# Optimization experiments

Hardware: AMD Instinct MI355X
Metric: run time of the kernel (lower is better)

## Reference

```python
import jax, jax.numpy as jnp
import numpy as np

EPS = 1e-5  # eqx.nn.LayerNorm default


def _layer_norm(x, w, b):
    m = x.mean(-1, keepdims=True)
    v = ((x - m) ** 2).mean(-1, keepdims=True)
    return (x - m) / jnp.sqrt(v + EPS) * w + b


def _s4_block(x, nw, nb, lre, lim, bre, bim, cre, cim, d, lstep, ow, ob, o2w, o2b):
    # x: [L, H]. One SequenceBlock: LayerNorm -> S4 recurrence (lax.scan) -> GELU -> GLU-style gated linear -> residual.
    skip = x
    h = _layer_norm(x, nw, nb)
    Lam = lre + 1j * lim                      # [H, N] complex diagonal state matrix
    step = jnp.exp(lstep)[:, None]            # [H, 1] per-channel timescale
    BL = 1.0 / (1.0 - (step / 2.0) * Lam)     # bilinear discretization
    Abar = BL * (1.0 + (step / 2.0) * Lam)    # [H, N]
    Bbar = BL * step * (bre + 1j * bim)       # [H, N]
    C = cre + 1j * cim                        # [H, N]

    def scan_fn(state, u):                    # state: [H, N] complex, u: [H]
        new = Abar * state + Bbar * u[:, None]
        y = 2.0 * jnp.sum(C * new, axis=-1).real + d * u
        return new, y

    init = jnp.zeros(Abar.shape, Abar.dtype)  # cell.init_state
    _, y = jax.lax.scan(scan_fn, init, h)     # [L, H]
    y = jax.nn.gelu(y)
    y = (y @ ow.T + ob) * jax.nn.sigmoid(y @ o2w.T + o2b)
    return skip + y


def setup_inputs() -> dict:
    key = jax.random.key(0)
    L, IN, OUT, H, N, NL = 2048, 4, 3, 512, 32, 4
    ks = jax.random.split(key, 16)
    return {
        "x": jax.random.normal(ks[0], (L, IN), jnp.float32),
        "enc_w": jax.random.normal(ks[1], (H, IN), jnp.float32) / np.sqrt(IN),
        "enc_b": jnp.zeros((H,), jnp.float32),
        "dec_w": jax.random.normal(ks[2], (OUT, H), jnp.float32) / np.sqrt(H),
        "dec_b": jnp.zeros((OUT,), jnp.float32),
        "norm_w": jnp.ones((NL, H), jnp.float32),
        "norm_b": jnp.zeros((NL, H), jnp.float32),
        "lam_re": -0.5 - jax.random.uniform(ks[3], (NL, H, N), jnp.float32),  # stable (Re < 0)
        "lam_im": np.pi * jax.random.normal(ks[4], (NL, H, N), jnp.float32),
        "b_re": jax.random.normal(ks[5], (NL, H, N), jnp.float32) / np.sqrt(N),
        "b_im": jax.random.normal(ks[6], (NL, H, N), jnp.float32) / np.sqrt(N),
        "c_re": jax.random.normal(ks[7], (NL, H, N), jnp.float32) / np.sqrt(N),
        "c_im": jax.random.normal(ks[8], (NL, H, N), jnp.float32) / np.sqrt(N),
        "d": jax.random.normal(ks[9], (NL, H), jnp.float32),
        "log_step": float(np.log(1e-3)) + float(np.log(1e-1) - np.log(1e-3)) * jax.random.uniform(ks[10], (NL, H), jnp.float32),
        "out_w": jax.random.normal(ks[11], (NL, H, H), jnp.float32) / np.sqrt(H),
        "out_b": jnp.zeros((NL, H), jnp.float32),
        "out2_w": jax.random.normal(ks[12], (NL, H, H), jnp.float32) / np.sqrt(H),
        "out2_b": jnp.zeros((NL, H), jnp.float32),
    }


def reference(x, enc_w, enc_b, dec_w, dec_b, norm_w, norm_b, lam_re, lam_im, b_re, b_im, c_re, c_im, d, log_step, out_w, out_b, out2_w, out2_b):
    h = x @ enc_w.T + enc_b                   # encoder: [L, IN] -> [L, H]
    for i in range(norm_w.shape[0]):          # fixed small n_layers loop
        h = _s4_block(h, norm_w[i], norm_b[i], lam_re[i], lam_im[i], b_re[i], b_im[i],
                      c_re[i], c_im[i], d[i], log_step[i], out_w[i], out_b[i], out2_w[i], out2_b[i])
    return h @ dec_w.T + dec_b                # decoder: [L, H] -> [L, OUT]
```

## Files before the change

kernel.cpp:

```cpp
#include <hip/hip_runtime.h>
#include <hip/hip_bf16.h>
#include <math.h>

#define LSEQ 2048
#define HD   512
#define NST  32
#define LC   32
#define NCHK 64
#define HH   (HD * HD)
#define NTHR 256

typedef __bf16 bf16;
typedef __bf16 bf16x8 __attribute__((ext_vector_type(8)));
typedef float  floatx4 __attribute__((ext_vector_type(4)));

__device__ __forceinline__ float wave_reduce_add(float v) {
#pragma unroll
    for (int m = 32; m; m >>= 1) v += __shfl_xor(v, m, 64);
    return v;
}

__device__ __forceinline__ float gelu_tanh(float x) {
    float z = 0.7978845608028654f * (x + 0.044715f * x * x * x);
    float e = __expf(2.f * z);
    float th = 1.f - 2.f / (e + 1.f);
    return 0.5f * x * (1.f + th);
}

__device__ __forceinline__ void make_ab(float lre, float lim, float step,
                                        float br0, float bi0,
                                        float& ar, float& ai, float& br, float& bi) {
    float s2 = 0.5f * step;
    float dr = 1.f - s2 * lre, di = -s2 * lim;
    float inv = 1.f / (dr * dr + di * di);
    float blr = dr * inv, bli = -di * inv;
    float nr = 1.f + s2 * lre, ni = s2 * lim;
    ar = blr * nr - bli * ni;
    ai = blr * ni + bli * nr;
    float tr = step * br0, ti = step * bi0;
    br = blr * tr - bli * ti;
    bi = blr * ti + bli * tr;
}

__global__ __launch_bounds__(256) void setup_kernel(
    const float* __restrict__ x,   const float* __restrict__ ew,
    const float* __restrict__ eb,  const float* __restrict__ ow,
    const float* __restrict__ o2w,
    const float* __restrict__ lre, const float* __restrict__ lim,
    const float* __restrict__ bre, const float* __restrict__ bim,
    const float* __restrict__ cre, const float* __restrict__ cim,
    const float* __restrict__ ls,
    float* __restrict__ h, bf16* __restrict__ wb,
    float2* __restrict__ cA, float2* __restrict__ cB,
    float2* __restrict__ cC, float2* __restrict__ cAp) {
    int bid = blockIdx.x, tid = threadIdx.x;
    if (bid < 4096) {
        int idx = bid * 256 + tid;
        int t = idx >> 9, i = idx & (HD - 1);
        float4 xv = *(const float4*)(x + t * 4);
        float4 wv = *(const float4*)(ew + i * 4);
        float acc = eb[i];
        acc = fmaf(xv.x, wv.x, acc); acc = fmaf(xv.y, wv.y, acc);
        acc = fmaf(xv.z, wv.z, acc); acc = fmaf(xv.w, wv.w, acc);
        h[idx] = acc;
    } else if (bid < 5120) {
        int b2 = bid - 4096;
        const float* src = (b2 >= 512) ? o2w : ow;
        bf16* dst = wb + (b2 >= 512 ? 4 * HH : 0);
        int i = ((b2 & 511) * 256 + tid) * 8;
        float4 a = *(const float4*)(src + i);
        float4 b = *(const float4*)(src + i + 4);
        bf16x8 o;
        o[0] = (bf16)a.x; o[1] = (bf16)a.y; o[2] = (bf16)a.z; o[3] = (bf16)a.w;
        o[4] = (bf16)b.x; o[5] = (bf16)b.y; o[6] = (bf16)b.z; o[7] = (bf16)b.w;
        *(bf16x8*)(dst + i) = o;
    } else {
        int tg = (bid - 5120) * 256 + tid;
        int lay = tg >> 14, rem = tg & 16383;
        int ch = rem >> 5, n = rem & 31;
        float step = __expf(ls[lay * HD + ch]);
        float ar, ai, br, bi;
        make_ab(lre[tg], lim[tg], step, bre[tg], bim[tg], ar, ai, br, bi);
        float xr = ar, xi = ai;
#pragma unroll
        for (int q = 0; q < 5; ++q) { float tt = xr * xr - xi * xi; xi = 2.f * xr * xi; xr = tt; }
        int dst = (lay * NST + n) * HD + ch;
        cA[dst]  = make_float2(ar, ai);
        cB[dst]  = make_float2(br, bi);
        cC[dst]  = make_float2(2.f * cre[tg], 2.f * cim[tg]);
        cAp[dst] = make_float2(xr, xi);
    }
}

__global__ __launch_bounds__(256) void lnstat_kernel(
    const float* __restrict__ h, float2* __restrict__ stats) {
    int wv = threadIdx.x >> 6, lane = threadIdx.x & 63;
    int row = blockIdx.x * 4 + wv;
    const float* hp = h + (size_t)row * HD + lane * 8;
    float v[8];
    *(float4*)(v)     = *(const float4*)(hp);
    *(float4*)(v + 4) = *(const float4*)(hp + 4);
    float s = 0.f;
#pragma unroll
    for (int e = 0; e < 8; ++e) s += v[e];
    s = wave_reduce_add(s);
    float m = s * (1.f / HD);
    float q = 0.f;
#pragma unroll
    for (int e = 0; e < 8; ++e) { float d = v[e] - m; q += d * d; }
    q = wave_reduce_add(q);
    float rstd = rsqrtf(q * (1.f / HD) + 1e-5f);
    if (lane == 0) stats[row] = make_float2(m, rstd);
}

__device__ __forceinline__ void load_norm_tile(
    float* tile, const float* __restrict__ h, const float2* __restrict__ stats,
    const float* __restrict__ nwp, const float* __restrict__ nbp,
    int bx, int by, int tid) {
    const float* ub = h + (size_t)(by * 4 * LC) * HD + bx * 16;
    const float2* st = stats + by * 4 * LC;
    const float* wp = nwp + bx * 16;
    const float* bp = nbp + bx * 16;
#pragma unroll
    for (int r = 0; r < 2; ++r) {
        int i = r * NTHR + tid;
        int tr = i >> 2, c4 = (i & 3) * 4;
        float4 hv = *(const float4*)(ub + (size_t)tr * HD + c4);
        float2 s2 = st[tr];
        float4 gv = *(const float4*)(wp + c4);
        float4 bv = *(const float4*)(bp + c4);
        float4 o;
        o.x = (hv.x - s2.x) * s2.y * gv.x + bv.x;
        o.y = (hv.y - s2.x) * s2.y * gv.y + bv.y;
        o.z = (hv.z - s2.x) * s2.y * gv.z + bv.z;
        o.w = (hv.w - s2.x) * s2.y * gv.w + bv.w;
        *(float4*)(tile + tr * 16 + c4) = o;
    }
}

__global__ __launch_bounds__(256, 2) void p1_kernel(
    const float* __restrict__ h, const float2* __restrict__ stats,
    const float* __restrict__ nwp, const float* __restrict__ nbp,
    const float2* __restrict__ cA, const float2* __restrict__ cB,
    float2* __restrict__ f, int lay) {
    __shared__ float tile[4 * LC * 16];
    int tid = threadIdx.x;
    int lane = tid & 63, w = tid >> 6;
    int chl = lane & 15, sub = lane >> 4;
    int bx = blockIdx.x, by = blockIdx.y;
    int ch = bx * 16 + chl;
    int chunk = by * 4 + w;
    load_norm_tile(tile, h, stats, nwp, nbp, bx, by, tid);
    int cbase = (lay * NST + sub * 8) * HD + ch;
    float aR[8], aI[8], bR[8], bI[8];
#pragma unroll
    for (int j = 0; j < 8; ++j) {
        float2 t = cA[cbase + j * HD]; aR[j] = t.x; aI[j] = t.y;
        t = cB[cbase + j * HD];        bR[j] = t.x; bI[j] = t.y;
    }
    float sr[8], si[8];
#pragma unroll
    for (int j = 0; j < 8; ++j) { sr[j] = 0.f; si[j] = 0.f; }
    __syncthreads();
    const float* tp = tile + (w * LC) * 16 + chl;
#pragma unroll 4
    for (int t = 0; t < LC; ++t) {
        float uu = tp[t * 16];
#pragma unroll
        for (int j = 0; j < 8; ++j) {
            float nr = fmaf(aR[j], sr[j], fmaf(-aI[j], si[j], bR[j] * uu));
            float ni = fmaf(aI[j], sr[j], fmaf( aR[j], si[j], bI[j] * uu));
            sr[j] = nr; si[j] = ni;
        }
    }
    float2* fp = f + (size_t)(chunk * NST + sub * 8) * HD + ch;
#pragma unroll
    for (int j = 0; j < 8; ++j) fp[(size_t)j * HD] = make_float2(sr[j], si[j]);
}

__global__ __launch_bounds__(256) void p2_kernel(
    float2* __restrict__ f, const float2* __restrict__ cAp, int lay) {
    int tg = blockIdx.x * 256 + threadIdx.x;
    int ch = tg & 511, n = tg >> 9;
    float2 ap = cAp[(lay * NST + n) * HD + ch];
    float2* fp = f + (size_t)n * HD + ch;
    const size_t cs = (size_t)NST * HD;
    float sr = 0.f, si = 0.f;
#pragma unroll 8
    for (int c = 0; c < NCHK; ++c) {
        float2 v = fp[c * cs];
        float nr = fmaf(ap.x, sr, fmaf(-ap.y, si, v.x));
        float ni = fmaf(ap.y, sr, fmaf( ap.x, si, v.y));
        sr = nr; si = ni;
        fp[c * cs] = make_float2(sr, si);
    }
}

__global__ __launch_bounds__(256, 2) void p3_kernel(
    const float* __restrict__ h, const float2* __restrict__ stats,
    const float* __restrict__ nwp, const float* __restrict__ nbp,
    const float2* __restrict__ f,
    const float2* __restrict__ cA, const float2* __restrict__ cB,
    const float2* __restrict__ cC, const float* __restrict__ d_p,
    bf16* __restrict__ g, int lay) {
    __shared__ float tile[4 * LC * 16];
    int tid = threadIdx.x;
    int lane = tid & 63, w = tid >> 6;
    int chl = lane & 15, sub = lane >> 4;
    int bx = blockIdx.x, by = blockIdx.y;
    int ch = bx * 16 + chl;
    int chunk = by * 4 + w;
    load_norm_tile(tile, h, stats, nwp, nbp, bx, by, tid);
    int cbase = (lay * NST + sub * 8) * HD + ch;
    float aR[8], aI[8], bR[8], bI[8], cR[8], cI[8];
#pragma unroll
    for (int j = 0; j < 8; ++j) {
        float2 t = cA[cbase + j * HD]; aR[j] = t.x; aI[j] = t.y;
        t = cB[cbase + j * HD];        bR[j] = t.x; bI[j] = t.y;
        t = cC[cbase + j * HD];        cR[j] = t.x; cI[j] = t.y;
    }
    float dch = d_p[lay * HD + ch];
    float sr[8], si[8];
    if (chunk > 0) {
        const float2* ip = f + (size_t)((chunk - 1) * NST + sub * 8) * HD + ch;
#pragma unroll
        for (int j = 0; j < 8; ++j) { float2 v = ip[(size_t)j * HD]; sr[j] = v.x; si[j] = v.y; }
    } else {
#pragma unroll
        for (int j = 0; j < 8; ++j) { sr[j] = 0.f; si[j] = 0.f; }
    }
    __syncthreads();
    const float* tp = tile + (w * LC) * 16 + chl;
    bf16* gp = g + (size_t)chunk * LC * HD + ch;
#pragma unroll 4
    for (int t = 0; t < LC; ++t) {
        float uu = tp[t * 16];
        float p = 0.f;
#pragma unroll
        for (int j = 0; j < 8; ++j) {
            float nr = fmaf(aR[j], sr[j], fmaf(-aI[j], si[j], bR[j] * uu));
            float ni = fmaf(aI[j], sr[j], fmaf( aR[j], si[j], bI[j] * uu));
            sr[j] = nr; si[j] = ni;
            p = fmaf(cR[j], nr, fmaf(-cI[j], ni, p));
        }
        p += __shfl_xor(p, 16);
        p += __shfl_xor(p, 32);
        float y = fmaf(dch, uu, p);
        if (sub == 0) gp[(size_t)t * HD] = (bf16)gelu_tanh(y);
    }
}

__global__ __launch_bounds__(256, 2) void mm_kernel(
    const bf16* __restrict__ A,
    const bf16* __restrict__ W1,
    const bf16* __restrict__ W2,
    const float* __restrict__ bias1, const float* __restrict__ bias2,
    float* __restrict__ Hio) {
    const int w = threadIdx.x >> 6, lane = threadIdx.x & 63;
    const int wm = w >> 1, wn = w & 1;
    const int bm = blockIdx.x >> 4, bn = blockIdx.x & 15;
    const int mW = bm * 64 + wm * 32;
    const int nW = bn * 32 + wn * 16;
    const int lrow = lane & 15, quad = lane >> 4;

    floatx4 acc1[2] = {{0.f,0.f,0.f,0.f},{0.f,0.f,0.f,0.f}};
    floatx4 acc2[2] = {{0.f,0.f,0.f,0.f},{0.f,0.f,0.f,0.f}};
    for (int k0 = 0; k0 < HD; k0 += 32) {
        int kk = k0 + quad * 8;
        bf16x8 a0 = *(const bf16x8*)(A + (size_t)(mW + lrow) * HD + kk);
        bf16x8 a1 = *(const bf16x8*)(A + (size_t)(mW + 16 + lrow) * HD + kk);
        bf16x8 p0 = *(const bf16x8*)(W1 + (size_t)(nW + lrow) * HD + kk);
        bf16x8 q0 = *(const bf16x8*)(W2 + (size_t)(nW + lrow) * HD + kk);
        acc1[0] = __builtin_amdgcn_mfma_f32_16x16x32_bf16(a0, p0, acc1[0], 0, 0, 0);
        acc1[1] = __builtin_amdgcn_mfma_f32_16x16x32_bf16(a1, p0, acc1[1], 0, 0, 0);
        acc2[0] = __builtin_amdgcn_mfma_f32_16x16x32_bf16(a0, q0, acc2[0], 0, 0, 0);
        acc2[1] = __builtin_amdgcn_mfma_f32_16x16x32_bf16(a1, q0, acc2[1], 0, 0, 0);
    }
    int jj = nW + lrow;
    float bb1 = bias1[jj], bb2 = bias2[jj];
#pragma unroll
    for (int fm = 0; fm < 2; ++fm)
#pragma unroll
        for (int r = 0; r < 4; ++r) {
            int t = mW + fm * 16 + quad * 4 + r;
            float z1 = acc1[fm][r] + bb1;
            float z2 = acc2[fm][r] + bb2;
            Hio[(size_t)t * HD + jj] += z1 / (1.f + __expf(-z2));
        }
}

__global__ __launch_bounds__(192) void dec_kernel(
    const float* __restrict__ h, const float* __restrict__ w,
    const float* __restrict__ b, float* __restrict__ out) {
    int j = threadIdx.x >> 6, lane = threadIdx.x & 63;
    int t = blockIdx.x;
    const float* hp = h + (size_t)t * HD + lane * 8;
    float v[8];
    *(float4*)(v)     = *(const float4*)(hp);
    *(float4*)(v + 4) = *(const float4*)(hp + 4);
    float w8[8];
    *(float4*)(w8)     = *(const float4*)(w + j * HD + lane * 8);
    *(float4*)(w8 + 4) = *(const float4*)(w + j * HD + lane * 8 + 4);
    float s = 0.f;
#pragma unroll
    for (int e = 0; e < 8; ++e) s = fmaf(v[e], w8[e], s);
    s = wave_reduce_add(s);
    if (lane == 0) out[t * 3 + j] = s + b[j];
}

extern "C" void kernel_launch(void* const* d_in, const int* in_sizes, int n_in,
                              void* d_out, int out_size, void* d_ws, size_t ws_size,
                              hipStream_t stream) {
    const float* x   = (const float*)d_in[0];
    const float* ew  = (const float*)d_in[1];
    const float* eb  = (const float*)d_in[2];
    const float* dw  = (const float*)d_in[3];
    const float* db  = (const float*)d_in[4];
    const float* nw  = (const float*)d_in[5];
    const float* nb  = (const float*)d_in[6];
    const float* lre = (const float*)d_in[7];
    const float* lim = (const float*)d_in[8];
    const float* bre = (const float*)d_in[9];
    const float* bim = (const float*)d_in[10];
    const float* cre = (const float*)d_in[11];
    const float* cim = (const float*)d_in[12];
    const float* dd  = (const float*)d_in[13];
    const float* ls  = (const float*)d_in[14];
    const float* ow  = (const float*)d_in[15];
    const float* ob  = (const float*)d_in[16];
    const float* o2w = (const float*)d_in[17];
    const float* o2b = (const float*)d_in[18];

    char* ws = (char*)d_ws;
    float*  h     = (float*)ws;
    float2* f     = (float2*)(ws + (4  << 20));
    bf16*   g     = (bf16*)(ws + (16 << 20));
    bf16*   wb    = (bf16*)(ws + (18 << 20));
    float2* cA    = (float2*)(ws + (22 << 20));
    float2* cB    = (float2*)(ws + (22 << 20) + (512 << 10));
    float2* cC    = (float2*)(ws + (23 << 20));
    float2* cAp   = (float2*)(ws + (23 << 20) + (512 << 10));
    float2* stats = (float2*)(ws + (24 << 20));

    setup_kernel<<<5376, 256, 0, stream>>>(x, ew, eb, ow, o2w,
                                           lre, lim, bre, bim, cre, cim, ls,
                                           h, wb, cA, cB, cC, cAp);
    for (int lay = 0; lay < 4; ++lay) {
        int oH = lay * HD;
        lnstat_kernel<<<LSEQ / 4, 256, 0, stream>>>(h, stats);
        p1_kernel<<<dim3(HD / 16, NCHK / 4), 256, 0, stream>>>(
            h, stats, nw + oH, nb + oH, cA, cB, f, lay);
        p2_kernel<<<64, 256, 0, stream>>>(f, cAp, lay);
        p3_kernel<<<dim3(HD / 16, NCHK / 4), 256, 0, stream>>>(
            h, stats, nw + oH, nb + oH, f, cA, cB, cC, dd, g, lay);
        mm_kernel<<<512, 256, 0, stream>>>(
            g, wb + lay * HH, wb + 4 * HH + lay * HH, ob + oH, o2b + oH, h);
    }
    dec_kernel<<<LSEQ, 192, 0, stream>>>(h, dw, db, (float*)d_out);
}
```

Measured before the change: 305.6 us.

## Fuse LayerNorm statistics into producer epilogues and prefetch p2 chunk loads

```diff
diff --git a/kernel.cpp b/kernel.cpp
--- a/kernel.cpp
+++ b/kernel.cpp
@@ -13,12 +13,6 @@
 typedef __bf16 bf16;
 typedef __bf16 bf16x8 __attribute__((ext_vector_type(8)));
 typedef float  floatx4 __attribute__((ext_vector_type(4)));
-
-__device__ __forceinline__ float wave_reduce_add(float v) {
-#pragma unroll
-    for (int m = 32; m; m >>= 1) v += __shfl_xor(v, m, 64);
-    return v;
-}
 
 __device__ __forceinline__ float gelu_tanh(float x) {
     float z = 0.7978845608028654f * (x + 0.044715f * x * x * x);
@@ -52,17 +46,25 @@
     const float* __restrict__ ls,
     float* __restrict__ h, bf16* __restrict__ wb,
     float2* __restrict__ cA, float2* __restrict__ cB,
-    float2* __restrict__ cC, float2* __restrict__ cAp) {
+    float2* __restrict__ cC, float2* __restrict__ cAp,
+    float2* __restrict__ statP) {
     int bid = blockIdx.x, tid = threadIdx.x;
     if (bid < 4096) {
         int idx = bid * 256 + tid;
-        int t = idx >> 9, i = idx & (HD - 1);
+        int t = idx >> 9, col = idx & (HD - 1);
         float4 xv = *(const float4*)(x + t * 4);
-        float4 wv = *(const float4*)(ew + i * 4);
-        float acc = eb[i];
+        float4 wv = *(const float4*)(ew + col * 4);
+        float acc = eb[col];
         acc = fmaf(xv.x, wv.x, acc); acc = fmaf(xv.y, wv.y, acc);
         acc = fmaf(xv.z, wv.z, acc); acc = fmaf(xv.w, wv.w, acc);
         h[idx] = acc;
+        float s = acc, s2 = acc * acc;
+#pragma unroll
+        for (int m = 1; m <= 8; m <<= 1) {
+            s  += __shfl_xor(s, m, 64);
+            s2 += __shfl_xor(s2, m, 64);
+        }
+        if ((tid & 15) == 0) statP[(size_t)t * 32 + (col >> 4)] = make_float2(s, s2);
     } else if (bid < 5120) {
         int b2 = bid - 4096;
         const float* src = (b2 >= 512) ? o2w : ow;
@@ -92,33 +94,25 @@
     }
 }
 
-__global__ __launch_bounds__(256) void lnstat_kernel(
-    const float* __restrict__ h, float2* __restrict__ stats) {
-    int wv = threadIdx.x >> 6, lane = threadIdx.x & 63;
-    int row = blockIdx.x * 4 + wv;
-    const float* hp = h + (size_t)row * HD + lane * 8;
-    float v[8];
-    *(float4*)(v)     = *(const float4*)(hp);
-    *(float4*)(v + 4) = *(const float4*)(hp + 4);
-    float s = 0.f;
-#pragma unroll
-    for (int e = 0; e < 8; ++e) s += v[e];
-    s = wave_reduce_add(s);
-    float m = s * (1.f / HD);
-    float q = 0.f;
-#pragma unroll
-    for (int e = 0; e < 8; ++e) { float d = v[e] - m; q += d * d; }
-    q = wave_reduce_add(q);
-    float rstd = rsqrtf(q * (1.f / HD) + 1e-5f);
-    if (lane == 0) stats[row] = make_float2(m, rstd);
-}
-
-__device__ __forceinline__ void load_norm_tile(
-    float* tile, const float* __restrict__ h, const float2* __restrict__ stats,
+__device__ __forceinline__ void stats_and_tile(
+    float* tile, float2* stat_s,
+    const float* __restrict__ h, const float2* __restrict__ statP,
     const float* __restrict__ nwp, const float* __restrict__ nbp,
     int bx, int by, int tid) {
+    if (tid < 128) {
+        const float4* pp = (const float4*)(statP + (size_t)(by * 128 + tid) * 32);
+        float S = 0.f, S2 = 0.f;
+#pragma unroll
+        for (int k = 0; k < 16; ++k) {
+            float4 v = pp[k];
+            S += v.x + v.z; S2 += v.y + v.w;
+        }
+        float m = S * (1.f / HD);
+        float var = S2 * (1.f / HD) - m * m;
+        stat_s[tid] = make_float2(m, rsqrtf(var + 1e-5f));
+    }
+    __syncthreads();
     const float* ub = h + (size_t)(by * 4 * LC) * HD + bx * 16;
-    const float2* st = stats + by * 4 * LC;
     const float* wp = nwp + bx * 16;
     const float* bp = nbp + bx * 16;
 #pragma unroll
@@ -126,7 +120,7 @@
         int i = r * NTHR + tid;
         int tr = i >> 2, c4 = (i & 3) * 4;
         float4 hv = *(const float4*)(ub + (size_t)tr * HD + c4);
-        float2 s2 = st[tr];
+        float2 s2 = stat_s[tr];
         float4 gv = *(const float4*)(wp + c4);
         float4 bv = *(const float4*)(bp + c4);
         float4 o;
@@ -139,18 +133,19 @@
 }
 
 __global__ __launch_bounds__(256, 2) void p1_kernel(
-    const float* __restrict__ h, const float2* __restrict__ stats,
+    const float* __restrict__ h, const float2* __restrict__ statP,
     const float* __restrict__ nwp, const float* __restrict__ nbp,
     const float2* __restrict__ cA, const float2* __restrict__ cB,
     float2* __restrict__ f, int lay) {
     __shared__ float tile[4 * LC * 16];
+    __shared__ float2 stat_s[128];
     int tid = threadIdx.x;
     int lane = tid & 63, w = tid >> 6;
     int chl = lane & 15, sub = lane >> 4;
     int bx = blockIdx.x, by = blockIdx.y;
     int ch = bx * 16 + chl;
     int chunk = by * 4 + w;
-    load_norm_tile(tile, h, stats, nwp, nbp, bx, by, tid);
+    stats_and_tile(tile, stat_s, h, statP, nwp, nbp, bx, by, tid);
     int cbase = (lay * NST + sub * 8) * HD + ch;
     float aR[8], aI[8], bR[8], bI[8];
 #pragma unroll
@@ -184,33 +179,45 @@
     int ch = tg & 511, n = tg >> 9;
     float2 ap = cAp[(lay * NST + n) * HD + ch];
     float2* fp = f + (size_t)n * HD + ch;
-    const size_t cs = (size_t)NST * HD;
+    const size_t CS = (size_t)NST * HD;
+    float2 cur[8], nxt[8];
+#pragma unroll
+    for (int k = 0; k < 8; ++k) cur[k] = fp[(size_t)k * CS];
     float sr = 0.f, si = 0.f;
-#pragma unroll 8
-    for (int c = 0; c < NCHK; ++c) {
-        float2 v = fp[c * cs];
-        float nr = fmaf(ap.x, sr, fmaf(-ap.y, si, v.x));
-        float ni = fmaf(ap.y, sr, fmaf( ap.x, si, v.y));
-        sr = nr; si = ni;
-        fp[c * cs] = make_float2(sr, si);
+#pragma unroll
+    for (int b = 0; b < 8; ++b) {
+        if (b < 7) {
+#pragma unroll
+            for (int k = 0; k < 8; ++k) nxt[k] = fp[(size_t)(b * 8 + 8 + k) * CS];
+        }
+#pragma unroll
+        for (int k = 0; k < 8; ++k) {
+            float nr = fmaf(ap.x, sr, fmaf(-ap.y, si, cur[k].x));
+            float ni = fmaf(ap.y, sr, fmaf( ap.x, si, cur[k].y));
+            sr = nr; si = ni;
+            fp[(size_t)(b * 8 + k) * CS] = make_float2(sr, si);
+        }
+#pragma unroll
+        for (int k = 0; k < 8; ++k) cur[k] = nxt[k];
     }
 }
 
 __global__ __launch_bounds__(256, 2) void p3_kernel(
-    const float* __restrict__ h, const float2* __restrict__ stats,
+    const float* __restrict__ h, const float2* __restrict__ statP,
     const float* __restrict__ nwp, const float* __restrict__ nbp,
     const float2* __restrict__ f,
     const float2* __restrict__ cA, const float2* __restrict__ cB,
     const float2* __restrict__ cC, const float* __restrict__ d_p,
     bf16* __restrict__ g, int lay) {
     __shared__ float tile[4 * LC * 16];
+    __shared__ float2 stat_s[128];
     int tid = threadIdx.x;
     int lane = tid & 63, w = tid >> 6;
     int chl = lane & 15, sub = lane >> 4;
     int bx = blockIdx.x, by = blockIdx.y;
     int ch = bx * 16 + chl;
     int chunk = by * 4 + w;
-    load_norm_tile(tile, h, stats, nwp, nbp, bx, by, tid);
+    stats_and_tile(tile, stat_s, h, statP, nwp, nbp, bx, by, tid);
     int cbase = (lay * NST + sub * 8) * HD + ch;
     float aR[8], aI[8], bR[8], bI[8], cR[8], cI[8];
 #pragma unroll
@@ -255,7 +262,7 @@
     const bf16* __restrict__ W1,
     const bf16* __restrict__ W2,
     const float* __restrict__ bias1, const float* __restrict__ bias2,
-    float* __restrict__ Hio) {
+    float* __restrict__ Hio, float2* __restrict__ statP, int doStats) {
     const int w = threadIdx.x >> 6, lane = threadIdx.x & 63;
     const int wm = w >> 1, wn = w & 1;
     const int bm = blockIdx.x >> 4, bn = blockIdx.x & 15;
@@ -278,6 +285,7 @@
     }
     int jj = nW + lrow;
     float bb1 = bias1[jj], bb2 = bias2[jj];
+    float hn_[2][4];
 #pragma unroll
     for (int fm = 0; fm < 2; ++fm)
 #pragma unroll
@@ -285,8 +293,27 @@
             int t = mW + fm * 16 + quad * 4 + r;
             float z1 = acc1[fm][r] + bb1;
             float z2 = acc2[fm][r] + bb2;
-            Hio[(size_t)t * HD + jj] += z1 / (1.f + __expf(-z2));
-        }
+            float v = Hio[(size_t)t * HD + jj] + z1 / (1.f + __expf(-z2));
+            Hio[(size_t)t * HD + jj] = v;
+            hn_[fm][r] = v;
+        }
+    if (doStats) {
+#pragma unroll
+        for (int fm = 0; fm < 2; ++fm)
+#pragma unroll
+            for (int r = 0; r < 4; ++r) {
+                float s = hn_[fm][r], s2 = s * s;
+#pragma unroll
+                for (int m = 1; m <= 8; m <<= 1) {
+                    s  += __shfl_xor(s, m, 64);
+                    s2 += __shfl_xor(s2, m, 64);
+                }
+                if (lrow == 0) {
+                    int t = mW + fm * 16 + quad * 4 + r;
+                    statP[(size_t)t * 32 + (nW >> 4)] = make_float2(s, s2);
+                }
+            }
+    }
 }
 
 __global__ __launch_bounds__(192) void dec_kernel(
@@ -304,7 +331,8 @@
     float s = 0.f;
 #pragma unroll
     for (int e = 0; e < 8; ++e) s = fmaf(v[e], w8[e], s);
-    s = wave_reduce_add(s);
+#pragma unroll
+    for (int m = 32; m; m >>= 1) s += __shfl_xor(s, m, 64);
     if (lane == 0) out[t * 3 + j] = s + b[j];
 }
 
@@ -340,21 +368,21 @@
     float2* cB    = (float2*)(ws + (22 << 20) + (512 << 10));
     float2* cC    = (float2*)(ws + (23 << 20));
     float2* cAp   = (float2*)(ws + (23 << 20) + (512 << 10));
-    float2* stats = (float2*)(ws + (24 << 20));
+    float2* statP = (float2*)(ws + (24 << 20));
 
     setup_kernel<<<5376, 256, 0, stream>>>(x, ew, eb, ow, o2w,
                                            lre, lim, bre, bim, cre, cim, ls,
-                                           h, wb, cA, cB, cC, cAp);
+                                           h, wb, cA, cB, cC, cAp, statP);
     for (int lay = 0; lay < 4; ++lay) {
         int oH = lay * HD;
-        lnstat_kernel<<<LSEQ / 4, 256, 0, stream>>>(h, stats);
         p1_kernel<<<dim3(HD / 16, NCHK / 4), 256, 0, stream>>>(
-            h, stats, nw + oH, nb + oH, cA, cB, f, lay);
+            h, statP, nw + oH, nb + oH, cA, cB, f, lay);
         p2_kernel<<<64, 256, 0, stream>>>(f, cAp, lay);
         p3_kernel<<<dim3(HD / 16, NCHK / 4), 256, 0, stream>>>(
-            h, stats, nw + oH, nb + oH, f, cA, cB, cC, dd, g, lay);
+            h, statP, nw + oH, nb + oH, f, cA, cB, cC, dd, g, lay);
         mm_kernel<<<512, 256, 0, stream>>>(
-            g, wb + lay * HH, wb + 4 * HH + lay * HH, ob + oH, o2b + oH, h);
+            g, wb + lay * HH, wb + 4 * HH + lay * HH, ob + oH, o2b + oH, h,
+            statP, lay < 3 ? 1 : 0);
     }
     dec_kernel<<<LSEQ, 192, 0, stream>>>(h, dw, db, (float*)d_out);
 }
```

Measured after the change: 305.4 us, median of 2. Within noise of the previous version (-0.1%).
